# Kernel optimization log

Measured on AMD Instinct MI355X. Metric: run time of the kernel, lower is better.

## Reference

```python
import math
import jax, jax.numpy as jnp
import numpy as np

N, T, C, V = 32, 2048, 512, 500


def setup_inputs() -> dict:
    key = jax.random.key(0)
    k1, k2, k3 = jax.random.split(key, 3)
    x = jax.random.normal(k1, (N, T, C), dtype=jnp.float32)
    x_lens = jax.random.randint(k2, (N,), 0, T, dtype=jnp.int64)
    ctc_output = jax.random.normal(k3, (N, T, V), dtype=jnp.float32)
    return {"x": x, "x_lens": x_lens, "ctc_output": ctc_output, "blank_id": 0}


def reference(x, x_lens, ctc_output, blank_id):
    # x: [N, T, C]; ctc_output: [N, T, V]; x_lens: [N]
    n, t, c = x.shape
    frame_idx = jnp.arange(t)  # [T]
    padding_mask = frame_idx[None, :] >= x_lens[:, None]              # [N, T]
    left = ctc_output[:, :, blank_id] < math.log(0.9)                 # blank posterior threshold
    non_blank_mask = left & (~padding_mask)                           # [N, T]
    out_lens = non_blank_mask.sum(axis=1)                             # [N]

    # Stable compaction: sort keep-frames (False < True on discard flag)
    # to the front of each row, preserving temporal order.
    order = jnp.argsort(~non_blank_mask, axis=1, stable=True)         # [N, T]
    out = jnp.take_along_axis(x, order[:, :, None], axis=1)           # [N, T, C]

    # Zero positions past each row's reduced length (original pads with zeros).
    valid = frame_idx[None, :] < out_lens[:, None]                    # [N, T]
    out = out * valid[:, :, None].astype(x.dtype)
    # Note: kept static-padded to T (jit-safe); original slices to out_lens.max().
    return out, out_lens
```

## Files before the change

### kernel.cpp

```cpp
#include <hip/hip_runtime.h>
#include <hip/hip_bf16.h>

#define RN 32
#define RT 2048
#define RC 512
#define RV 500

#define LOG09 (-0.10536052f)

__global__ void fr_mask_scan(const float* __restrict__ ctc,
                             const int* __restrict__ x_lens,
                             const int* __restrict__ blank_id_p,
                             int* __restrict__ src_idx,
                             int* __restrict__ lens_i,
                             float* __restrict__ lens_f)
{
    const int n   = blockIdx.x;
    const int tid = threadIdx.x;
    const int blank = blank_id_p[0];
    const int xlen  = x_lens[n];

    const float* row = ctc + (size_t)n * RT * RV;
    const int base = tid * 8;

    unsigned flags = 0;
    int cnt = 0;
#pragma unroll
    for (int j = 0; j < 8; ++j) {
        const int t = base + j;
        const bool keep = (t < xlen) && (row[(size_t)t * RV + blank] < LOG09);
        flags |= (keep ? 1u : 0u) << j;
        cnt += keep ? 1 : 0;
    }

    __shared__ int s[256];
    s[tid] = cnt;
    __syncthreads();
#pragma unroll
    for (int off = 1; off < 256; off <<= 1) {
        int v = 0;
        if (tid >= off) v = s[tid - off];
        __syncthreads();
        if (tid >= off) s[tid] += v;
        __syncthreads();
    }
    const int excl  = s[tid] - cnt;
    const int total = s[255];

    int* srow = src_idx + n * RT;
    int pos = excl;
#pragma unroll
    for (int j = 0; j < 8; ++j) {
        if ((flags >> j) & 1u) {
            srow[pos++] = base + j;
        }
    }

    if (tid == 0) {
        lens_i[n] = total;
        lens_f[n] = (float)total;
    }
}

__global__ void fr_gather(const float* __restrict__ x,
                          const int* __restrict__ src_idx,
                          const int* __restrict__ lens_i,
                          float4* __restrict__ out)
{
    const int r    = blockIdx.x * 2 + (threadIdx.x >> 7);
    const int lane = threadIdx.x & 127;
    const int n = r >> 11;
    const int p = r & (RT - 1);

    float4 v = make_float4(0.f, 0.f, 0.f, 0.f);
    if (p < lens_i[n]) {
        const int t = src_idx[n * RT + p];
        const float4* xr = (const float4*)(x + ((size_t)n * RT + t) * RC);
        v = xr[lane];
    }
    out[(size_t)r * (RC / 4) + lane] = v;
}

extern "C" void kernel_launch(void* const* d_in, const int* in_sizes, int n_in,
                              void* d_out, int out_size, void* d_ws, size_t ws_size,
                              hipStream_t stream) {
    const float* x        = (const float*)d_in[0];
    const int*   x_lens   = (const int*)d_in[1];
    const float* ctc      = (const float*)d_in[2];
    const int*   blank_id = (const int*)d_in[3];

    float* out    = (float*)d_out;
    float* lens_f = out + (size_t)RN * RT * RC;

    int* src_idx = (int*)d_ws;
    int* lens_i  = src_idx + RN * RT;

    fr_mask_scan<<<RN, 256, 0, stream>>>(ctc, x_lens, blank_id, src_idx, lens_i, lens_f);
    fr_gather<<<(RN * RT) / 2, 256, 0, stream>>>(x, src_idx, lens_i, (float4*)out);
}
```

Measured before the change: 34.03 us.

## Split mask scan into grid-wide ballot flag kernel and wavefront scan

The single 32-block mask/scan kernel is replaced by two kernels. A 256-block kernel reads one blank logit per thread and packs keep flags into 64-bit words with wavefront ballot. A second, one-wave-per-row kernel does a popcount plus shuffle prefix scan and writes the compacted indices. This spreads the strided, latency-bound ctc reads over many more CUs, at the cost of an extra kernel launch and serial per-lane index writes.

After: 36.13 us. 6.2% more time.

```diff
diff --git a/kernel.cpp b/kernel.cpp
--- a/kernel.cpp
+++ b/kernel.cpp
@@ -8,55 +8,59 @@
 
 #define LOG09 (-0.10536052f)
 
-__global__ void fr_mask_scan(const float* __restrict__ ctc,
-                             const int* __restrict__ x_lens,
-                             const int* __restrict__ blank_id_p,
-                             int* __restrict__ src_idx,
-                             int* __restrict__ lens_i,
-                             float* __restrict__ lens_f)
+__global__ void fr_flags(const float* __restrict__ ctc,
+                         const int* __restrict__ x_lens,
+                         const int* __restrict__ blank_id_p,
+                         unsigned long long* __restrict__ flag_words)
 {
-    const int n   = blockIdx.x;
-    const int tid = threadIdx.x;
+    const int g = blockIdx.x * 256 + threadIdx.x;
+    const int n = g >> 11;
+    const int t = g & (RT - 1);
     const int blank = blank_id_p[0];
-    const int xlen  = x_lens[n];
 
-    const float* row = ctc + (size_t)n * RT * RV;
-    const int base = tid * 8;
+    const bool keep = (t < x_lens[n]) &&
+                      (ctc[(size_t)g * RV + blank] < LOG09);
+    const unsigned long long b = __ballot(keep);
+    if ((threadIdx.x & 63) == 0) {
+        flag_words[g >> 6] = b;
+    }
+}
 
-    unsigned flags = 0;
+__global__ void fr_scan(const unsigned long long* __restrict__ flag_words,
+                        int* __restrict__ src_idx,
+                        int* __restrict__ lens_i,
+                        float* __restrict__ lens_f)
+{
+    const int n    = blockIdx.x;
+    const int lane = threadIdx.x;
+
+    unsigned long long word = 0;
     int cnt = 0;
-#pragma unroll
-    for (int j = 0; j < 8; ++j) {
-        const int t = base + j;
-        const bool keep = (t < xlen) && (row[(size_t)t * RV + blank] < LOG09);
-        flags |= (keep ? 1u : 0u) << j;
-        cnt += keep ? 1 : 0;
+    if (lane < 32) {
+        word = flag_words[n * 32 + lane];
+        cnt  = __popcll(word);
     }
 
-    __shared__ int s[256];
-    s[tid] = cnt;
-    __syncthreads();
+    int incl = cnt;
 #pragma unroll
-    for (int off = 1; off < 256; off <<= 1) {
-        int v = 0;
-        if (tid >= off) v = s[tid - off];
-        __syncthreads();
-        if (tid >= off) s[tid] += v;
-        __syncthreads();
+    for (int off = 1; off < 32; off <<= 1) {
+        int v = __shfl_up(incl, off, 64);
+        if (lane >= off) incl += v;
     }
-    const int excl  = s[tid] - cnt;
-    const int total = s[255];
+    const int total = __shfl(incl, 31, 64);
 
-    int* srow = src_idx + n * RT;
-    int pos = excl;
-#pragma unroll
-    for (int j = 0; j < 8; ++j) {
-        if ((flags >> j) & 1u) {
+    if (lane < 32) {
+        int pos = incl - cnt;
+        int* srow = src_idx + n * RT;
+        const int base = lane * 64;
+        unsigned long long w = word;
+        while (w) {
+            const int j = __ffsll((long long)w) - 1;
             srow[pos++] = base + j;
+            w &= w - 1;
         }
     }
-
-    if (tid == 0) {
+    if (lane == 0) {
         lens_i[n] = total;
         lens_f[n] = (float)total;
     }
@@ -94,7 +98,10 @@
 
     int* src_idx = (int*)d_ws;
     int* lens_i  = src_idx + RN * RT;
+    unsigned long long* flag_words =
+        (unsigned long long*)(lens_i + RN + (RN & 1));
 
-    fr_mask_scan<<<RN, 256, 0, stream>>>(ctc, x_lens, blank_id, src_idx, lens_i, lens_f);
+    fr_flags<<<(RN * RT) / 256, 256, 0, stream>>>(ctc, x_lens, blank_id, flag_words);
+    fr_scan<<<RN, 64, 0, stream>>>(flag_words, src_idx, lens_i, lens_f);
     fr_gather<<<(RN * RT) / 2, 256, 0, stream>>>(x, src_idx, lens_i, (float4*)out);
 }
```

## Use wave ballot scan for compaction and multi-row gather with nontemporal stores

Applied to the files above, without the earlier changes.

The scan kernel now runs 1024 threads per row, with each thread loading two blank posteriors. Prefix sums are built from wave ballots and popcounts instead of a shared-memory Hillis-Steele scan, and padded slots get -1 sentinels so the separate length array is gone. The gather kernel has each wave copy 8 rows with two float4 loads per lane per row, prefetches the next index, and writes the output with nontemporal stores. The aim is less scan latency and fewer gather blocks, at the cost of fewer waves in flight for the gather.

Result: slower. 38.94 us (+14.4%).

```diff
diff --git a/kernel.cpp b/kernel.cpp
--- a/kernel.cpp
+++ b/kernel.cpp
@@ -8,77 +8,95 @@
 
 #define LOG09 (-0.10536052f)
 
-__global__ void fr_mask_scan(const float* __restrict__ ctc,
-                             const int* __restrict__ x_lens,
-                             const int* __restrict__ blank_id_p,
-                             int* __restrict__ src_idx,
-                             int* __restrict__ lens_i,
-                             float* __restrict__ lens_f)
+typedef unsigned long long ull;
+typedef float v4f __attribute__((ext_vector_type(4)));
+
+__global__ __launch_bounds__(1024)
+void fr_mask_scan(const float* __restrict__ ctc,
+                  const int* __restrict__ x_lens,
+                  const int* __restrict__ blank_id_p,
+                  int* __restrict__ src_idx,
+                  float* __restrict__ lens_f)
 {
-    const int n   = blockIdx.x;
-    const int tid = threadIdx.x;
+    const int n    = blockIdx.x;
+    const int tid  = threadIdx.x;
+    const int wid  = tid >> 6;
+    const int lane = tid & 63;
     const int blank = blank_id_p[0];
     const int xlen  = x_lens[n];
 
-    const float* row = ctc + (size_t)n * RT * RV;
-    const int base = tid * 8;
+    const float* row = ctc + (size_t)n * RT * RV + blank;
 
-    unsigned flags = 0;
-    int cnt = 0;
+    const int t0 = wid * 128 + lane;
+    const int t1 = t0 + 64;
+    const bool k0 = (t0 < xlen) && (row[(size_t)t0 * RV] < LOG09);
+    const bool k1 = (t1 < xlen) && (row[(size_t)t1 * RV] < LOG09);
+    const ull w0 = __ballot(k0);
+    const ull w1 = __ballot(k1);
+    const int c0 = __popcll(w0);
+    const int wcnt = c0 + __popcll(w1);
+
+    __shared__ int sh_cnt[16];
+    __shared__ int sh_excl[16];
+    __shared__ int sh_total;
+
+    if (lane == 0) sh_cnt[wid] = wcnt;
+    __syncthreads();
+    if (tid < 16) {
+        int incl = sh_cnt[tid];
 #pragma unroll
-    for (int j = 0; j < 8; ++j) {
-        const int t = base + j;
-        const bool keep = (t < xlen) && (row[(size_t)t * RV + blank] < LOG09);
-        flags |= (keep ? 1u : 0u) << j;
-        cnt += keep ? 1 : 0;
+        for (int off = 1; off < 16; off <<= 1) {
+            int v = __shfl_up(incl, off, 64);
+            if (tid >= off) incl += v;
+        }
+        sh_excl[tid] = incl - sh_cnt[tid];
+        if (tid == 15) sh_total = incl;
     }
+    __syncthreads();
 
-    __shared__ int s[256];
-    s[tid] = cnt;
-    __syncthreads();
-#pragma unroll
-    for (int off = 1; off < 256; off <<= 1) {
-        int v = 0;
-        if (tid >= off) v = s[tid - off];
-        __syncthreads();
-        if (tid >= off) s[tid] += v;
-        __syncthreads();
-    }
-    const int excl  = s[tid] - cnt;
-    const int total = s[255];
+    const int total = sh_total;
+    int* srow = src_idx + n * RT;
 
-    int* srow = src_idx + n * RT;
-    int pos = excl;
-#pragma unroll
-    for (int j = 0; j < 8; ++j) {
-        if ((flags >> j) & 1u) {
-            srow[pos++] = base + j;
-        }
-    }
+    const ull ltmask = ((ull)1 << lane) - 1;
+    const int base = sh_excl[wid];
+    if (k0) srow[base + __popcll(w0 & ltmask)] = t0;
+    if (k1) srow[base + c0 + __popcll(w1 & ltmask)] = t1;
 
-    if (tid == 0) {
-        lens_i[n] = total;
-        lens_f[n] = (float)total;
-    }
+    if (t0 >= total) srow[t0] = -1;
+    if (t1 >= total) srow[t1] = -1;
+
+    if (tid == 0) lens_f[n] = (float)total;
 }
 
-__global__ void fr_gather(const float* __restrict__ x,
-                          const int* __restrict__ src_idx,
-                          const int* __restrict__ lens_i,
-                          float4* __restrict__ out)
+__global__ __launch_bounds__(256)
+void fr_gather(const float* __restrict__ x,
+               const int* __restrict__ src_idx,
+               float* __restrict__ out)
 {
-    const int r    = blockIdx.x * 2 + (threadIdx.x >> 7);
-    const int lane = threadIdx.x & 127;
-    const int n = r >> 11;
-    const int p = r & (RT - 1);
+    const int gwid = (blockIdx.x * 256 + threadIdx.x) >> 6;
+    const int lane = threadIdx.x & 63;
+    const int row_base = gwid * 8;
+    const int n = row_base >> 11;
+    const int p0 = row_base & (RT - 1);
 
-    float4 v = make_float4(0.f, 0.f, 0.f, 0.f);
-    if (p < lens_i[n]) {
-        const int t = src_idx[n * RT + p];
-        const float4* xr = (const float4*)(x + ((size_t)n * RT + t) * RC);
-        v = xr[lane];
+    const v4f* xb = (const v4f*)x + (size_t)n * RT * (RC / 4);
+    v4f* ob = (v4f*)out + (size_t)(n * RT + p0) * (RC / 4);
+    const int* sp = src_idx + n * RT + p0;
+
+    int t = sp[0];
+#pragma unroll
+    for (int r = 0; r < 8; ++r) {
+        const int t_next = (r < 7) ? sp[r + 1] : 0;
+        v4f v0 = (v4f)(0.f);
+        v4f v1 = (v4f)(0.f);
+        if (t >= 0) {
+            v0 = xb[(size_t)t * (RC / 4) + lane];
+            v1 = xb[(size_t)t * (RC / 4) + 64 + lane];
+        }
+        __builtin_nontemporal_store(v0, &ob[(size_t)r * (RC / 4) + lane]);
+        __builtin_nontemporal_store(v1, &ob[(size_t)r * (RC / 4) + 64 + lane]);
+        t = t_next;
     }
-    out[(size_t)r * (RC / 4) + lane] = v;
 }
 
 extern "C" void kernel_launch(void* const* d_in, const int* in_sizes, int n_in,
@@ -93,8 +111,7 @@
     float* lens_f = out + (size_t)RN * RT * RC;
 
     int* src_idx = (int*)d_ws;
-    int* lens_i  = src_idx + RN * RT;
 
-    fr_mask_scan<<<RN, 256, 0, stream>>>(ctc, x_lens, blank_id, src_idx, lens_i, lens_f);
-    fr_gather<<<(RN * RT) / 2, 256, 0, stream>>>(x, src_idx, lens_i, (float4*)out);
+    fr_mask_scan<<<RN, 1024, 0, stream>>>(ctc, x_lens, blank_id, src_idx, lens_f);
+    fr_gather<<<(RN * RT) / 32, 256, 0, stream>>>(x, src_idx, out);
 }
```
